# Kernel optimization log

Measured on AMD Instinct MI355X. Metric: run time of the kernel, lower is better.

Reference implementation:

```python
import jax, jax.numpy as jnp
import numpy as np

EPS = 1e-12  # matches torch F.normalize clamp_min eps
SCALE = 20.0
NEG = -1e9


def l2norm(x):
    return x / jnp.maximum(jnp.linalg.norm(x, axis=-1, keepdims=True), EPS)


def setup_inputs() -> dict:
    key = jax.random.key(0)
    B, P, A, DV, DT, E = 32, 192, 30, 768, 768, 256
    ks = jax.random.split(key, 8)
    visual_feature = jax.random.normal(ks[0], (B, 1 + P, DV), jnp.float32)
    textual_feature = jax.random.normal(ks[1], (B, 1 + A, DT), jnp.float32)
    att_nums = jax.random.randint(ks[2], (B,), 1, A + 1)  # valid attr counts >=1
    # mask==1 marks padded attribute slots (consistent with att_nums)
    mask = (jnp.arange(A)[None, :] >= att_nums[:, None]).astype(jnp.int32)
    W_vis = 0.02 * jax.random.normal(ks[3], (E, DV), jnp.float32)
    W_txt = 0.02 * jax.random.normal(ks[4], (E, DT), jnp.float32)
    W_patch = 0.02 * jax.random.normal(ks[5], (E, DV), jnp.float32)
    W_att = 0.02 * jax.random.normal(ks[6], (E, DT), jnp.float32)
    z = jnp.zeros((E,), jnp.float32)
    return {
        "visual_feature": visual_feature, "textual_feature": textual_feature,
        "mask": mask, "att_nums": att_nums,
        "W_vis": W_vis, "b_vis": z, "W_txt": W_txt, "b_txt": z,
        "W_patch": W_patch, "b_patch": z, "W_att": W_att, "b_att": z,
    }


def reference(visual_feature, textual_feature, mask, att_nums,
              W_vis, b_vis, W_txt, b_txt, W_patch, b_patch, W_att, b_att):
    # token splits + linear projections
    visual_embed = visual_feature[:, 0] @ W_vis.T + b_vis        # [Bv, E]
    patch = visual_feature[:, 1:] @ W_patch.T + b_patch           # [Bv, P, E]
    textual_embed = textual_feature[:, 0] @ W_txt.T + b_txt       # [Bt, E]
    att = textual_feature[:, 1:] @ W_att.T + b_att                # [Bt, A, E]

    pad = mask.astype(bool)                                       # [Bt, A], True = padded

    # attention 1: each text's attributes attend over every image's patches
    s1 = jax.nn.relu(jnp.einsum('tae,vpe->vtap', l2norm(att), l2norm(patch))) * SCALE
    attn1 = jax.nn.softmax(s1, axis=-1)                           # [Bv, Bt, A, P]
    attend_patch = jnp.einsum('vtap,vpe->vtae', attn1, patch)     # [Bv, Bt, A, E]
    attend_patch = jnp.where(pad[None, :, :, None], 0.0, attend_patch)

    # attention 2: each image's patches attend over every text's attributes (masked)
    s2 = jax.nn.relu(jnp.einsum('vpe,tae->tvpa', l2norm(patch), l2norm(att))) * SCALE
    s2 = jnp.where(pad[:, None, None, :], NEG, s2)                # [Bt, Bv, P, A]
    attn2 = jax.nn.softmax(s2, axis=-1)
    attend_att = jnp.einsum('tvpa,tae->tvpe', attn2, att)         # [Bt, Bv, P, E]

    # local similarity
    ap = l2norm(attend_patch)                                     # [Bv, Bt, A, E]
    aa = l2norm(attend_att)                                       # [Bt, Bv, P, E]
    an = att_nums.astype(aa.dtype)
    sim = jnp.einsum('tvpe,vtae->tvpa', aa, ap) / an[:, None, None, None]
    local_similarity = sim.sum(axis=2).mean(axis=2)               # [Bt, Bv]

    # training-path global embeds
    patch_mean = patch.mean(axis=1)                               # [Bv, E]
    att_mean = (att / an[:, None, None]).sum(axis=1)              # [Bt, E]

    return (visual_embed, textual_embed, patch_mean, att_mean, local_similarity)
```

## Files before the change

### kernel.cpp

```cpp
#include <hip/hip_runtime.h>
#include <math.h>

#define D_IN 768
#define E_DIM 256
#define NB 32
#define NP 192
#define NA 30

typedef __attribute__((ext_vector_type(8))) __bf16 bf16x8;
typedef __attribute__((ext_vector_type(4))) float f32x4;

__global__ __launch_bounds__(256) void proj_fused_kernel(
    const float* __restrict__ vf, const float* __restrict__ tf,
    const float* __restrict__ Wv, const float* __restrict__ bv,
    const float* __restrict__ Wt, const float* __restrict__ bt,
    const float* __restrict__ Wp, const float* __restrict__ bp,
    const float* __restrict__ Wa, const float* __restrict__ ba,
    const int* __restrict__ att_nums,
    float* __restrict__ out_vis, float* __restrict__ out_txt,
    float* __restrict__ out_pm, float* __restrict__ out_am,
    __bf16* __restrict__ pn_frag, __bf16* __restrict__ pB_frag,
    __bf16* __restrict__ an_frag, __bf16* __restrict__ attT_frag)
{
    __shared__ __align__(16) unsigned char smem[36864];
    __bf16* As = (__bf16*)smem;
    __bf16* Bs = (__bf16*)(smem + 4096);
    float*  LDSf = (float*)smem;
    __shared__ float invn_s[32];

    const int bid = blockIdx.x;
    const int tid = threadIdx.x;
    const int w = tid >> 6, l = tid & 63, q = l >> 4, n15 = l & 15;

    int role;
    const float *W, *bias;
    if (bid < 192)       { role = 0; W = Wp; bias = bp; }
    else if (bid < 224)  { role = 1; W = Wa; bias = ba; }
    else if (bid == 224) { role = 2; W = Wv; bias = bv; }
    else                 { role = 3; W = Wt; bias = bt; }

    const int rl = tid >> 3, oct = tid & 7;
    const float* arow;
    if (role == 0) {
        const int r = bid * 32 + rl;
        const int b = r / NP, idx = r - b * NP;
        arow = vf + (size_t)(b * 193 + 1 + idx) * D_IN;
    } else if (role == 1) {
        const int t = bid - 192;
        const int rr = (rl < NA) ? rl : 0;
        arow = tf + (size_t)(t * 31 + 1 + rr) * D_IN;
    } else if (role == 2) {
        arow = vf + (size_t)rl * 193 * D_IN;
    } else {
        arow = tf + (size_t)rl * 31 * D_IN;
    }
    const float* wrow = W + (size_t)tid * D_IN;
    const int et = tid >> 4, elo = tid & 15;

    f32x4 acc[2][4];
    #pragma unroll
    for (int m = 0; m < 2; ++m)
        #pragma unroll
        for (int n = 0; n < 4; ++n) { f32x4 z = {0.f,0.f,0.f,0.f}; acc[m][n] = z; }

    for (int kk = 0; kk < D_IN; kk += 64) {
        __syncthreads();
        {
            float4 f0 = *(const float4*)&arow[kk + oct * 8];
            float4 f1 = *(const float4*)&arow[kk + oct * 8 + 4];
            bf16x8 vv;
            vv[0]=(__bf16)f0.x; vv[1]=(__bf16)f0.y; vv[2]=(__bf16)f0.z; vv[3]=(__bf16)f0.w;
            vv[4]=(__bf16)f1.x; vv[5]=(__bf16)f1.y; vv[6]=(__bf16)f1.z; vv[7]=(__bf16)f1.w;
            const int mt = rl >> 4, koct = oct >> 2;
            *(bf16x8*)&As[(((mt * 2 + koct) * 64) + (rl & 15) + 16 * (oct & 3)) * 8] = vv;
        }
        #pragma unroll
        for (int o = 0; o < 8; ++o) {
            float4 f0 = *(const float4*)&wrow[kk + o * 8];
            float4 f1 = *(const float4*)&wrow[kk + o * 8 + 4];
            bf16x8 vv;
            vv[0]=(__bf16)f0.x; vv[1]=(__bf16)f0.y; vv[2]=(__bf16)f0.z; vv[3]=(__bf16)f0.w;
            vv[4]=(__bf16)f1.x; vv[5]=(__bf16)f1.y; vv[6]=(__bf16)f1.z; vv[7]=(__bf16)f1.w;
            *(bf16x8*)&Bs[(((o >> 2) * 16 + et) * 64 + elo + 16 * (o & 3)) * 8] = vv;
        }
        __syncthreads();
        #pragma unroll
        for (int kq = 0; kq < 2; ++kq) {
            bf16x8 a0 = *(const bf16x8*)&As[((0 * 2 + kq) * 64 + l) * 8];
            bf16x8 a1 = *(const bf16x8*)&As[((1 * 2 + kq) * 64 + l) * 8];
            #pragma unroll
            for (int nt = 0; nt < 4; ++nt) {
                bf16x8 bf_ = *(const bf16x8*)&Bs[((kq * 16 + (w * 4 + nt)) * 64 + l) * 8];
                acc[0][nt] = __builtin_amdgcn_mfma_f32_16x16x32_bf16(a0, bf_, acc[0][nt], 0, 0, 0);
                acc[1][nt] = __builtin_amdgcn_mfma_f32_16x16x32_bf16(a1, bf_, acc[1][nt], 0, 0, 0);
            }
        }
    }
    __syncthreads();

    if (role >= 2) {
        float* outp = (role == 2) ? out_vis : out_txt;
        #pragma unroll
        for (int mt = 0; mt < 2; ++mt)
            #pragma unroll
            for (int nt = 0; nt < 4; ++nt) {
                const int col = (w * 4 + nt) * 16 + n15;
                const float b = bias[col];
                #pragma unroll
                for (int r = 0; r < 4; ++r) {
                    const int row = mt * 16 + q * 4 + r;
                    outp[row * E_DIM + col] = acc[mt][nt][r] + b;
                }
            }
        return;
    }

    #pragma unroll
    for (int mt = 0; mt < 2; ++mt)
        #pragma unroll
        for (int nt = 0; nt < 4; ++nt) {
            const int col = (w * 4 + nt) * 16 + n15;
            const float b = bias[col];
            #pragma unroll
            for (int r = 0; r < 4; ++r)
                LDSf[(mt * 16 + q * 4 + r) * 260 + col] = acc[mt][nt][r] + b;
        }
    __syncthreads();

    if (role == 0) {
        const int v = bid / 6, c = bid - 6 * v;
        {
            const int row = tid >> 3, seg = tid & 7;
            const float* rr = &LDSf[row * 260 + seg * 32];
            float ssq = 0.f;
            #pragma unroll
            for (int j = 0; j < 32; ++j) ssq += rr[j] * rr[j];
            ssq += __shfl_xor(ssq, 1, 64);
            ssq += __shfl_xor(ssq, 2, 64);
            ssq += __shfl_xor(ssq, 4, 64);
            if (seg == 0) invn_s[row] = 1.f / fmaxf(sqrtf(ssq), 1e-12f);
        }
        {
            float s = 0.f;
            #pragma unroll
            for (int r = 0; r < 32; ++r) s += LDSf[r * 260 + tid];
            atomicAdd(&out_pm[v * E_DIM + tid], s * (1.f / 192.f));
        }
        __syncthreads();
        __bf16* dstn = pn_frag + (size_t)(v * 6 + c) * 8192;
        #pragma unroll
        for (int i = 0; i < 4; ++i) {
            const int slot = tid + 256 * i;
            const int mt = slot >> 9, koct = (slot >> 6) & 7, lane = slot & 63;
            const int prl = mt * 16 + (lane & 15);
            const int e0 = koct * 32 + (lane >> 4) * 8;
            const float inr = invn_s[prl];
            const float* src = &LDSf[prl * 260 + e0];
            bf16x8 vv;
            #pragma unroll
            for (int j = 0; j < 8; ++j) vv[j] = (__bf16)(src[j] * inr);
            *(bf16x8*)&dstn[slot * 8] = vv;
        }
        __bf16* dstb = pB_frag + (size_t)(v * 6 + c) * 8192;
        #pragma unroll
        for (int i = 0; i < 4; ++i) {
            const int slot = tid + 256 * i;
            const int nt = slot >> 6, lane = slot & 63;
            const int e = nt * 16 + (lane & 15);
            const int p0 = (lane >> 4) * 8;
            bf16x8 vv;
            #pragma unroll
            for (int j = 0; j < 8; ++j) vv[j] = (__bf16)LDSf[(p0 + j) * 260 + e];
            *(bf16x8*)&dstb[slot * 8] = vv;
        }
    } else {
        const int t = bid - 192;
        const int Av = att_nums[t];
        {
            const int row = tid >> 3, seg = tid & 7;
            const float* rr = &LDSf[row * 260 + seg * 32];
            float ssq = 0.f;
            #pragma unroll
            for (int j = 0; j < 32; ++j) ssq += rr[j] * rr[j];
            ssq += __shfl_xor(ssq, 1, 64);
            ssq += __shfl_xor(ssq, 2, 64);
            ssq += __shfl_xor(ssq, 4, 64);
            if (seg == 0) invn_s[row] = (row < NA) ? 1.f / fmaxf(sqrtf(ssq), 1e-12f) : 0.f;
        }
        {
            float s = 0.f;
            #pragma unroll
            for (int r = 0; r < NA; ++r) s += LDSf[r * 260 + tid];
            out_am[t * E_DIM + tid] = s / (float)Av;
        }
        __syncthreads();
        __bf16* dstn = an_frag + (size_t)t * 8192;
        #pragma unroll
        for (int i = 0; i < 4; ++i) {
            const int slot = tid + 256 * i;
            const int at = slot >> 9, koct = (slot >> 6) & 7, lane = slot & 63;
            const int a = at * 16 + (lane & 15);
            const int e0 = koct * 32 + (lane >> 4) * 8;
            const float inr = (a < NA) ? invn_s[a] : 0.f;
            const float* src = &LDSf[a * 260 + e0];
            bf16x8 vv;
            #pragma unroll
            for (int j = 0; j < 8; ++j) vv[j] = (__bf16)(src[j] * inr);
            *(bf16x8*)&dstn[slot * 8] = vv;
        }
        __bf16* dstb = attT_frag + (size_t)t * 8192;
        #pragma unroll
        for (int i = 0; i < 4; ++i) {
            const int slot = tid + 256 * i;
            const int nt = slot >> 6, lane = slot & 63;
            const int e = nt * 16 + (lane & 15);
            const int a0 = (lane >> 4) * 8;
            bf16x8 vv;
            #pragma unroll
            for (int j = 0; j < 8; ++j)
                vv[j] = (a0 + j < NA) ? (__bf16)LDSf[(a0 + j) * 260 + e] : (__bf16)0.f;
            *(bf16x8*)&dstb[slot * 8] = vv;
        }
    }
}

__global__ __launch_bounds__(256) void pair_mfma_kernel(
    const __bf16* __restrict__ pn_frag, const __bf16* __restrict__ pB_frag,
    const __bf16* __restrict__ an_frag, const __bf16* __restrict__ attT_frag,
    const int* __restrict__ att_nums, float* __restrict__ out_sim)
{
    __shared__ __align__(16) __bf16 an_s[8192];
    __shared__ __align__(16) __bf16 attT_s[8192];
    __shared__ __align__(16) __bf16 pn_s[8192];
    __shared__ __align__(16) __bf16 pB_s[8192];
    __shared__ __align__(16) __bf16 Xa_s[1024];
    __shared__ __align__(16) __bf16 XaT_s[1024];
    __shared__ float red_s[128];
    __shared__ float invn_s[32];
    __shared__ float wred_s[4];

    const int v = blockIdx.x, t = blockIdx.y;
    const int tid = threadIdx.x;
    const int w = tid >> 6, l = tid & 63, q = l >> 4, n15 = l & 15;
    const int Av = att_nums[t];

    {
        const __bf16* s1 = an_frag + (size_t)t * 8192;
        const __bf16* s2 = attT_frag + (size_t)t * 8192;
        #pragma unroll
        for (int i = 0; i < 4; ++i) {
            const int slot = tid + 256 * i;
            *(bf16x8*)&an_s[slot * 8]   = *(const bf16x8*)&s1[slot * 8];
            *(bf16x8*)&attT_s[slot * 8] = *(const bf16x8*)&s2[slot * 8];
        }
    }
    __syncthreads();

    bf16x8 ab[4];
    #pragma unroll
    for (int n = 0; n < 4; ++n)
        ab[n] = *(const bf16x8*)&attT_s[((w * 4 + n) * 64 + l) * 8];

    f32x4 apacc[2][4];
    #pragma unroll
    for (int m = 0; m < 2; ++m)
        #pragma unroll
        for (int n = 0; n < 4; ++n) { f32x4 z = {0.f,0.f,0.f,0.f}; apacc[m][n] = z; }
    float sa_acc[4] = {0.f, 0.f, 0.f, 0.f};

    for (int c = 0; c < 6; ++c) {
        __syncthreads();
        {
            const __bf16* sp1 = pn_frag + (size_t)(v * 6 + c) * 8192;
            const __bf16* sp2 = pB_frag + (size_t)(v * 6 + c) * 8192;
            #pragma unroll
            for (int i = 0; i < 4; ++i) {
                const int slot = tid + 256 * i;
                *(bf16x8*)&pn_s[slot * 8] = *(const bf16x8*)&sp1[slot * 8];
                *(bf16x8*)&pB_s[slot * 8] = *(const bf16x8*)&sp2[slot * 8];
            }
        }
        __syncthreads();

        {
            const int mt = w >> 1, at = w & 1;
            f32x4 sacc = {0.f, 0.f, 0.f, 0.f};
            #pragma unroll
            for (int kp = 0; kp < 8; ++kp) {
                bf16x8 af  = *(const bf16x8*)&pn_s[((mt * 8 + kp) * 64 + l) * 8];
                bf16x8 bf_ = *(const bf16x8*)&an_s[((at * 8 + kp) * 64 + l) * 8];
                sacc = __builtin_amdgcn_mfma_f32_16x16x32_bf16(af, bf_, sacc, 0, 0, 0);
            }
            const int a = at * 16 + n15;
            #pragma unroll
            for (int r = 0; r < 4; ++r) {
                const int pcl = q * 4 + r;
                const int pcc = mt * 16 + pcl;
                float xvv = (a < Av) ? __expf(fmaxf(20.f * sacc[r], 0.f)) : 0.f;
                __bf16 h = (__bf16)xvv;
                Xa_s[mt * 512 + (pcl + 16 * (a >> 3)) * 8 + (a & 7)] = h;
                XaT_s[at * 512 + (n15 + 16 * (pcc >> 3)) * 8 + (pcc & 7)] = h;
            }
        }
        __syncthreads();

        f32x4 aacc[2][4];
        {
            bf16x8 xa0 = *(const bf16x8*)&Xa_s[l * 8];
            bf16x8 xa1 = *(const bf16x8*)&Xa_s[512 + l * 8];
            bf16x8 xt0 = *(const bf16x8*)&XaT_s[l * 8];
            bf16x8 xt1 = *(const bf16x8*)&XaT_s[512 + l * 8];
            #pragma unroll
            for (int n = 0; n < 4; ++n) {
                f32x4 z = {0.f, 0.f, 0.f, 0.f};
                aacc[0][n] = __builtin_amdgcn_mfma_f32_16x16x32_bf16(xa0, ab[n], z, 0, 0, 0);
                aacc[1][n] = __builtin_amdgcn_mfma_f32_16x16x32_bf16(xa1, ab[n], z, 0, 0, 0);
                bf16x8 pb = *(const bf16x8*)&pB_s[((w * 4 + n) * 64 + l) * 8];
                apacc[0][n] = __builtin_amdgcn_mfma_f32_16x16x32_bf16(xt0, pb, apacc[0][n], 0, 0, 0);
                apacc[1][n] = __builtin_amdgcn_mfma_f32_16x16x32_bf16(xt1, pb, apacc[1][n], 0, 0, 0);
            }
        }

        #pragma unroll
        for (int mt2 = 0; mt2 < 2; ++mt2)
            #pragma unroll
            for (int r = 0; r < 4; ++r) {
                float ssq = 0.f;
                #pragma unroll
                for (int n = 0; n < 4; ++n) { float vv = aacc[mt2][n][r]; ssq += vv * vv; }
                ssq += __shfl_xor(ssq, 1, 64);
                ssq += __shfl_xor(ssq, 2, 64);
                ssq += __shfl_xor(ssq, 4, 64);
                ssq += __shfl_xor(ssq, 8, 64);
                if (n15 == 0) red_s[(mt2 * 16 + q * 4 + r) * 4 + w] = ssq;
            }
        __syncthreads();
        if (tid < 32) {
            float s = red_s[tid * 4] + red_s[tid * 4 + 1] + red_s[tid * 4 + 2] + red_s[tid * 4 + 3];
            invn_s[tid] = 1.f / fmaxf(sqrtf(s), 1e-12f);
        }
        __syncthreads();
        #pragma unroll
        for (int mt2 = 0; mt2 < 2; ++mt2)
            #pragma unroll
            for (int r = 0; r < 4; ++r) {
                const float inr = invn_s[mt2 * 16 + q * 4 + r];
                #pragma unroll
                for (int n = 0; n < 4; ++n) sa_acc[n] += aacc[mt2][n][r] * inr;
            }
    }

    #pragma unroll
    for (int mt2 = 0; mt2 < 2; ++mt2)
        #pragma unroll
        for (int r = 0; r < 4; ++r) {
            float ssq = 0.f;
            #pragma unroll
            for (int n = 0; n < 4; ++n) { float vv = apacc[mt2][n][r]; ssq += vv * vv; }
            ssq += __shfl_xor(ssq, 1, 64);
            ssq += __shfl_xor(ssq, 2, 64);
            ssq += __shfl_xor(ssq, 4, 64);
            ssq += __shfl_xor(ssq, 8, 64);
            if (n15 == 0) red_s[(mt2 * 16 + q * 4 + r) * 4 + w] = ssq;
        }
    __syncthreads();
    if (tid < 32) {
        float s = red_s[tid * 4] + red_s[tid * 4 + 1] + red_s[tid * 4 + 2] + red_s[tid * 4 + 3];
        invn_s[tid] = 1.f / fmaxf(sqrtf(s), 1e-12f);
    }
    __syncthreads();

    float prod = 0.f;
    #pragma unroll
    for (int n = 0; n < 4; ++n) {
        float sp = 0.f;
        #pragma unroll
        for (int mt2 = 0; mt2 < 2; ++mt2)
            #pragma unroll
            for (int r = 0; r < 4; ++r)
                sp += apacc[mt2][n][r] * invn_s[mt2 * 16 + q * 4 + r];
        float saf = sa_acc[n];
        saf += __shfl_xor(saf, 16, 64);
        saf += __shfl_xor(saf, 32, 64);
        float spf = sp;
        spf += __shfl_xor(spf, 16, 64);
        spf += __shfl_xor(spf, 32, 64);
        prod += saf * spf;
    }
    prod += __shfl_xor(prod, 1, 64);
    prod += __shfl_xor(prod, 2, 64);
    prod += __shfl_xor(prod, 4, 64);
    prod += __shfl_xor(prod, 8, 64);
    prod += __shfl_xor(prod, 16, 64);
    prod += __shfl_xor(prod, 32, 64);
    if (l == 0) wred_s[w] = prod;
    __syncthreads();
    if (tid == 0)
        out_sim[t * NB + v] = (wred_s[0] + wred_s[1] + wred_s[2] + wred_s[3]) * 0.25f
                              / ((float)Av * 30.f);
}

extern "C" void kernel_launch(void* const* d_in, const int* in_sizes, int n_in,
                              void* d_out, int out_size, void* d_ws, size_t ws_size,
                              hipStream_t stream)
{
    const float* vf = (const float*)d_in[0];
    const float* tf = (const float*)d_in[1];
    const int*   an = (const int*)d_in[3];
    const float* Wv = (const float*)d_in[4];
    const float* bv = (const float*)d_in[5];
    const float* Wt = (const float*)d_in[6];
    const float* bt = (const float*)d_in[7];
    const float* Wp = (const float*)d_in[8];
    const float* bp = (const float*)d_in[9];
    const float* Wa = (const float*)d_in[10];
    const float* ba = (const float*)d_in[11];

    float* out = (float*)d_out;
    float* out_vis = out;
    float* out_txt = out + 8192;
    float* out_pm  = out + 16384;
    float* out_am  = out + 24576;
    float* out_sim = out + 32768;

    __bf16* wsb = (__bf16*)d_ws;
    __bf16* pn_frag   = wsb;
    __bf16* pB_frag   = wsb + 1572864;
    __bf16* an_frag   = wsb + 3145728;
    __bf16* attT_frag = wsb + 3407872;

    hipMemsetAsync((char*)d_out + 16384 * sizeof(float), 0, 8192 * sizeof(float), stream);

    proj_fused_kernel<<<226, 256, 0, stream>>>(
        vf, tf, Wv, bv, Wt, bt, Wp, bp, Wa, ba, an,
        out_vis, out_txt, out_pm, out_am,
        pn_frag, pB_frag, an_frag, attT_frag);

    pair_mfma_kernel<<<dim3(NB, NB), 256, 0, stream>>>(
        pn_frag, pB_frag, an_frag, attT_frag, an, out_sim);
}
```

Measured before the change: 163.4 us.

## Load MFMA operands directly from global memory, dropping LDS staging in projection GEMM

The projection GEMM no longer stages bf16-converted A and W tiles through shared memory with two barriers per K step. Each lane now loads its MFMA fragment straight from global fp32 rows, converts it to bf16 in registers, and issues the MFMAs. This removes the LDS round trip and the synchronisation. In exchange, W fragments are re-read from global memory or cache by every wave with less coalesced access, and the A rows are loaded redundantly across the four waves.

```diff
diff --git a/kernel.cpp b/kernel.cpp
--- a/kernel.cpp
+++ b/kernel.cpp
@@ -9,6 +9,13 @@
 
 typedef __attribute__((ext_vector_type(8))) __bf16 bf16x8;
 typedef __attribute__((ext_vector_type(4))) float f32x4;
+
+__device__ __forceinline__ bf16x8 cvt8(float4 a, float4 b) {
+    bf16x8 v;
+    v[0]=(__bf16)a.x; v[1]=(__bf16)a.y; v[2]=(__bf16)a.z; v[3]=(__bf16)a.w;
+    v[4]=(__bf16)b.x; v[5]=(__bf16)b.y; v[6]=(__bf16)b.z; v[7]=(__bf16)b.w;
+    return v;
+}
 
 __global__ __launch_bounds__(256) void proj_fused_kernel(
     const float* __restrict__ vf, const float* __restrict__ tf,
@@ -22,10 +29,7 @@
     __bf16* __restrict__ pn_frag, __bf16* __restrict__ pB_frag,
     __bf16* __restrict__ an_frag, __bf16* __restrict__ attT_frag)
 {
-    __shared__ __align__(16) unsigned char smem[36864];
-    __bf16* As = (__bf16*)smem;
-    __bf16* Bs = (__bf16*)(smem + 4096);
-    float*  LDSf = (float*)smem;
+    __shared__ float LDSf[32 * 260];
     __shared__ float invn_s[32];
 
     const int bid = blockIdx.x;
@@ -39,23 +43,28 @@
     else if (bid == 224) { role = 2; W = Wv; bias = bv; }
     else                 { role = 3; W = Wt; bias = bt; }
 
-    const int rl = tid >> 3, oct = tid & 7;
-    const float* arow;
+    const float *arow0, *arow1;
     if (role == 0) {
-        const int r = bid * 32 + rl;
-        const int b = r / NP, idx = r - b * NP;
-        arow = vf + (size_t)(b * 193 + 1 + idx) * D_IN;
+        const int v = bid / 6, c = bid - 6 * v;
+        arow0 = vf + (size_t)(v * 193 + 1 + c * 32 + n15) * D_IN;
+        arow1 = arow0 + (size_t)16 * D_IN;
     } else if (role == 1) {
         const int t = bid - 192;
-        const int rr = (rl < NA) ? rl : 0;
-        arow = tf + (size_t)(t * 31 + 1 + rr) * D_IN;
+        const int r0 = n15;
+        const int r1 = (16 + n15 < NA) ? 16 + n15 : 0;
+        arow0 = tf + (size_t)(t * 31 + 1 + r0) * D_IN;
+        arow1 = tf + (size_t)(t * 31 + 1 + r1) * D_IN;
     } else if (role == 2) {
-        arow = vf + (size_t)rl * 193 * D_IN;
+        arow0 = vf + (size_t)n15 * 193 * D_IN;
+        arow1 = vf + (size_t)(16 + n15) * 193 * D_IN;
     } else {
-        arow = tf + (size_t)rl * 31 * D_IN;
-    }
-    const float* wrow = W + (size_t)tid * D_IN;
-    const int et = tid >> 4, elo = tid & 15;
+        arow0 = tf + (size_t)n15 * 31 * D_IN;
+        arow1 = tf + (size_t)(16 + n15) * 31 * D_IN;
+    }
+    const float* wrow[4];
+    #pragma unroll
+    for (int nt = 0; nt < 4; ++nt)
+        wrow[nt] = W + (size_t)((w * 4 + nt) * 16 + n15) * D_IN;
 
     f32x4 acc[2][4];
     #pragma unroll
@@ -63,40 +72,25 @@
         #pragma unroll
         for (int n = 0; n < 4; ++n) { f32x4 z = {0.f,0.f,0.f,0.f}; acc[m][n] = z; }
 
-    for (int kk = 0; kk < D_IN; kk += 64) {
-        __syncthreads();
-        {
-            float4 f0 = *(const float4*)&arow[kk + oct * 8];
-            float4 f1 = *(const float4*)&arow[kk + oct * 8 + 4];
-            bf16x8 vv;
-            vv[0]=(__bf16)f0.x; vv[1]=(__bf16)f0.y; vv[2]=(__bf16)f0.z; vv[3]=(__bf16)f0.w;
-            vv[4]=(__bf16)f1.x; vv[5]=(__bf16)f1.y; vv[6]=(__bf16)f1.z; vv[7]=(__bf16)f1.w;
-            const int mt = rl >> 4, koct = oct >> 2;
-            *(bf16x8*)&As[(((mt * 2 + koct) * 64) + (rl & 15) + 16 * (oct & 3)) * 8] = vv;
-        }
-        #pragma unroll
-        for (int o = 0; o < 8; ++o) {
-            float4 f0 = *(const float4*)&wrow[kk + o * 8];
-            float4 f1 = *(const float4*)&wrow[kk + o * 8 + 4];
-            bf16x8 vv;
-            vv[0]=(__bf16)f0.x; vv[1]=(__bf16)f0.y; vv[2]=(__bf16)f0.z; vv[3]=(__bf16)f0.w;
-            vv[4]=(__bf16)f1.x; vv[5]=(__bf16)f1.y; vv[6]=(__bf16)f1.z; vv[7]=(__bf16)f1.w;
-            *(bf16x8*)&Bs[(((o >> 2) * 16 + et) * 64 + elo + 16 * (o & 3)) * 8] = vv;
-        }
-        __syncthreads();
-        #pragma unroll
-        for (int kq = 0; kq < 2; ++kq) {
-            bf16x8 a0 = *(const bf16x8*)&As[((0 * 2 + kq) * 64 + l) * 8];
-            bf16x8 a1 = *(const bf16x8*)&As[((1 * 2 + kq) * 64 + l) * 8];
-            #pragma unroll
-            for (int nt = 0; nt < 4; ++nt) {
-                bf16x8 bf_ = *(const bf16x8*)&Bs[((kq * 16 + (w * 4 + nt)) * 64 + l) * 8];
-                acc[0][nt] = __builtin_amdgcn_mfma_f32_16x16x32_bf16(a0, bf_, acc[0][nt], 0, 0, 0);
-                acc[1][nt] = __builtin_amdgcn_mfma_f32_16x16x32_bf16(a1, bf_, acc[1][nt], 0, 0, 0);
-            }
-        }
-    }
-    __syncthreads();
+    const int kq8 = q * 8;
+    #pragma unroll 4
+    for (int kt = 0; kt < 24; ++kt) {
+        const int k0 = kt * 32 + kq8;
+        float4 fa0 = *(const float4*)&arow0[k0];
+        float4 fa1 = *(const float4*)&arow0[k0 + 4];
+        float4 fb0 = *(const float4*)&arow1[k0];
+        float4 fb1 = *(const float4*)&arow1[k0 + 4];
+        bf16x8 a0 = cvt8(fa0, fa1);
+        bf16x8 a1 = cvt8(fb0, fb1);
+        #pragma unroll
+        for (int nt = 0; nt < 4; ++nt) {
+            float4 w0 = *(const float4*)&wrow[nt][k0];
+            float4 w1 = *(const float4*)&wrow[nt][k0 + 4];
+            bf16x8 bfr = cvt8(w0, w1);
+            acc[0][nt] = __builtin_amdgcn_mfma_f32_16x16x32_bf16(a0, bfr, acc[0][nt], 0, 0, 0);
+            acc[1][nt] = __builtin_amdgcn_mfma_f32_16x16x32_bf16(a1, bfr, acc[1][nt], 0, 0, 0);
+        }
+    }
 
     if (role >= 2) {
         float* outp = (role == 2) ? out_vis : out_txt;
```

New measurement: 176.0 us. 7.8% more time.
